# Kernel optimization log

Measured on AMD Instinct MI355X. Metric: run time of the kernel, lower is better.

## Reference

```python
import jax, jax.numpy as jnp
import numpy as np

B, CIN, H, W = 8, 128, 28, 28
COUT = 256
KH, KW, SH, SW, PH, PW = 3, 3, 1, 1, 1, 1
NCB, K = 64, 16
D = CIN * KH * KW          # 1152
SUB = D // NCB             # 18
OH = (H + 2 * PH - KH) // SH + 1
OW = (W + 2 * PW - KW) // SW + 1


def dequant(q, s, z):
    return (q.astype(jnp.float32) - z.astype(jnp.float32)) * s


def unfold(x):
    # x: (B, CIN, H, W) -> (B, D, OH*OW) with torch.unfold channel-major ordering
    xp = jnp.pad(x, ((0, 0), (0, 0), (PH, PH), (PW, PW)))
    patches = [xp[:, :, i:i + SH * OH:SH, j:j + SW * OW:SW]
               for i in range(KH) for j in range(KW)]
    cols = jnp.stack(patches, axis=2)  # (B, CIN, KH*KW, OH, OW)
    return cols.reshape(B, D, OH * OW)


def setup_inputs() -> dict:
    key = jax.random.key(0)
    ks = jax.random.split(key, 8)
    x_q = jax.random.randint(ks[0], (B, CIN, H, W), -128, 128, dtype=jnp.int32)
    x_s = jnp.array([0.02], jnp.float32)
    x_z = jnp.array([3], jnp.int32)
    centroids_q = jax.random.randint(ks[1], (NCB, K, SUB), -128, 128, dtype=jnp.int32)
    centroids_s = jax.random.uniform(ks[2], (NCB, 1, 1), jnp.float32) * 0.02 + 0.005
    centroids_z = jax.random.randint(ks[3], (NCB, 1, 1), -4, 5, dtype=jnp.int32)
    lut_q = jax.random.randint(ks[4], (NCB, K, COUT), -128, 128, dtype=jnp.int32)
    lut_s = jnp.array([0.015], jnp.float32)
    lut_z = jnp.array([1], jnp.int32)
    bias_q = jax.random.randint(ks[5], (COUT,), -1000, 1000, dtype=jnp.int32)
    bias_s = jnp.array([0.001], jnp.float32)
    bias_z = jnp.array([0], jnp.int32)
    output_s = jnp.array([0.05], jnp.float32)
    output_z = jnp.array([-2], jnp.int32)
    return dict(x_q=x_q, x_s=x_s, x_z=x_z,
                centroids_q=centroids_q, centroids_s=centroids_s, centroids_z=centroids_z,
                lut_q=lut_q, lut_s=lut_s, lut_z=lut_z,
                bias_q=bias_q, bias_s=bias_s, bias_z=bias_z,
                output_s=output_s, output_z=output_z)


def reference(x_q, x_s, x_z, centroids_q, centroids_s, centroids_z,
              lut_q, lut_s, lut_z, bias_q, bias_s, bias_z, output_s, output_z):
    x = dequant(x_q, x_s, x_z)                      # (B, CIN, H, W)
    cols = unfold(x)                                # (B, D, L)
    N = B * OH * OW
    # (B, L, D) -> (N, NCB, SUB) -> (NCB, N, SUB)
    xr = cols.transpose(0, 2, 1).reshape(N, NCB, SUB).transpose(1, 0, 2)
    c = dequant(centroids_q, centroids_s, centroids_z)  # (NCB, K, SUB)
    xy = jnp.einsum('cns,cks->cnk', xr, c)          # (NCB, N, K)
    y2 = jnp.sum(c * c, axis=-1)[:, None, :]        # (NCB, 1, K)
    den = x_s * centroids_s                         # (NCB, 1, 1)
    dist = -2.0 * jnp.round(xy / den) + jnp.round(y2 / den)
    idx = jnp.argmin(dist, axis=-1)                 # (NCB, N) int
    lut = dequant(lut_q, lut_s, lut_z)              # (NCB, K, COUT)
    # one_hot @ lut == gather rows of lut at idx, then sum over codebooks
    gathered = jnp.take_along_axis(lut, idx[:, :, None], axis=1)  # (NCB, N, COUT)
    out = jnp.sum(gathered, axis=0) + dequant(bias_q, bias_s, bias_z)  # (N, COUT)
    out = out.reshape(B, OH, OW, COUT).transpose(0, 3, 1, 2)
    out = jax.nn.relu(out)
    out_q = jnp.round(jnp.clip(out / output_s + output_z.astype(jnp.float32),
                               -128.0, 127.0)).astype(jnp.int8)
    return out_q
```

## Files before the change

kernel.cpp:

```cpp
#include <hip/hip_runtime.h>
#include <math.h>

constexpr int B_    = 8;
constexpr int CIN_  = 128;
constexpr int H_    = 28;
constexpr int W_    = 28;
constexpr int COUT_ = 256;
constexpr int OH_   = 28;
constexpr int OW_   = 28;
constexpr int L_    = OH_ * OW_;
constexpr int N_    = B_ * L_;
constexpr int NCB_  = 64;
constexpr int K_    = 16;
constexpr int SUB_  = 18;

constexpr size_t WS_IDX  = 0;
constexpr size_t WS_LUT8 = 0x100000;
constexpr size_t WS_BF2  = 0x180000;

__global__ __launch_bounds__(256, 2) void amm_k1(
    const int* __restrict__ x_q, const int* __restrict__ x_z,
    const int* __restrict__ c_q, const float* __restrict__ c_s,
    const int* __restrict__ c_z, const float* __restrict__ x_s,
    const int* __restrict__ lut_q, const float* __restrict__ lut_s,
    const int* __restrict__ lut_z,
    const int* __restrict__ bias_q, const float* __restrict__ bias_s,
    const int* __restrict__ bias_z,
    unsigned char* __restrict__ idx8, unsigned char* __restrict__ lut8,
    float* __restrict__ biasf2)
{
    const int bx  = blockIdx.x;
    const int tid = threadIdx.x;

    if (bx >= 512) {
        const int pb = bx - 512;
        if (pb < 256) {
            const int i = pb * 1024 + tid * 4;
            const int4 v = *(const int4*)(lut_q + i);
            uchar4 o;
            o.x = (unsigned char)(v.x + 128);
            o.y = (unsigned char)(v.y + 128);
            o.z = (unsigned char)(v.z + 128);
            o.w = (unsigned char)(v.w + 128);
            *(uchar4*)(lut8 + i) = o;
        } else {
            const double ls = (double)lut_s[0];
            const double c0 = (8192.0 + 64.0 * (double)lut_z[0]) * ls;
            biasf2[tid] = (float)((double)(bias_q[tid] - bias_z[0]) *
                                  (double)bias_s[0] - c0);
        }
        return;
    }

    const int cb = bx & 63;
    const int b  = bx >> 6;

    __shared__ float sx[2][900];
    __shared__ float c_lds[288];
    __shared__ float y2_lds[16];

    const int zc = c_z[cb];
    for (int i = tid; i < 1800; i += 256) ((float*)sx)[i] = 0.0f;
    for (int i = tid; i < 288; i += 256) {
        const int k = i / SUB_, s = i - k * SUB_;
        c_lds[s * 16 + k] = (float)(c_q[cb * 288 + i] - zc);
    }
    __syncthreads();

    const int xz = x_z[0];
    for (int i = tid; i < 2 * 784; i += 256) {
        const int c2 = i >= 784;
        const int r  = i - c2 * 784;
        const int h  = r / 28;
        const int w  = r - h * 28;
        sx[c2][(h + 1) * 30 + (w + 1)] =
            (float)(x_q[(size_t)(b * CIN_ + 2 * cb + c2) * L_ + r] - xz);
    }
    if (tid < 16) {
        const double csf = (double)c_s[cb];
        const double den = (double)x_s[0] * csf;
        double s2 = 0.0;
        for (int s = 0; s < SUB_; ++s) {
            const double d = (double)c_lds[s * 16 + tid] * csf;
            s2 += d * d;
        }
        y2_lds[tid] = (float)(int)rint(s2 / den);
    }
    __syncthreads();

    if (tid < 196) {
        float tap[4][SUB_];
        int   posr[4];
        #pragma unroll
        for (int ps = 0; ps < 4; ++ps) {
            const int p  = tid + 196 * ps;
            posr[ps] = p;
            const int oh = p / 28;
            const int ow = p - oh * 28;
            const int base = oh * 30 + ow;
            #pragma unroll
            for (int c2 = 0; c2 < 2; ++c2)
                #pragma unroll
                for (int kh = 0; kh < 3; ++kh)
                    #pragma unroll
                    for (int kw = 0; kw < 3; ++kw)
                        tap[ps][c2 * 9 + kh * 3 + kw] =
                            sx[c2][base + kh * 30 + kw];
        }

        float bestd[4] = {3.0e38f, 3.0e38f, 3.0e38f, 3.0e38f};
        int   bestk[4] = {0, 0, 0, 0};

        #pragma unroll
        for (int kc = 0; kc < 4; ++kc) {
            float acc[4][4];
            #pragma unroll
            for (int ps = 0; ps < 4; ++ps)
                #pragma unroll
                for (int kk = 0; kk < 4; ++kk) acc[ps][kk] = 0.0f;

            #pragma unroll
            for (int s = 0; s < SUB_; ++s) {
                const float4 c4 = *(const float4*)&c_lds[s * 16 + kc * 4];
                #pragma unroll
                for (int ps = 0; ps < 4; ++ps) {
                    const float xs = tap[ps][s];
                    acc[ps][0] = fmaf(xs, c4.x, acc[ps][0]);
                    acc[ps][1] = fmaf(xs, c4.y, acc[ps][1]);
                    acc[ps][2] = fmaf(xs, c4.z, acc[ps][2]);
                    acc[ps][3] = fmaf(xs, c4.w, acc[ps][3]);
                }
            }
            #pragma unroll
            for (int kk = 0; kk < 4; ++kk) {
                const float yk = y2_lds[kc * 4 + kk];
                #pragma unroll
                for (int ps = 0; ps < 4; ++ps) {
                    const float d = fmaf(-2.0f, acc[ps][kk], yk);
                    if (d < bestd[ps]) { bestd[ps] = d; bestk[ps] = kc * 4 + kk; }
                }
            }
        }

        unsigned char* op = idx8 + (size_t)cb * N_ + b * L_;
        #pragma unroll
        for (int ps = 0; ps < 4; ++ps)
            op[posr[ps]] = (unsigned char)bestk[ps];
    }
}

__global__ __launch_bounds__(256, 6) void amm_phase2(
    const unsigned char* __restrict__ idx8, const unsigned char* __restrict__ lut8,
    const float* __restrict__ lut_s, const float* __restrict__ biasf2,
    const float* __restrict__ out_s, const int* __restrict__ out_z,
    int* __restrict__ out)
{
    const int tid  = threadIdx.x;
    const int lane = tid & 63;
    const int wv   = __builtin_amdgcn_readfirstlane(tid >> 6);
    const int nb   = blockIdx.x * 4;
    const int b    = nb / L_;
    const int r0   = nb - b * L_;
    const int sh   = 8 * wv;

    __shared__ unsigned int sidx[64];
    __shared__ unsigned int res[4][132];

    if (tid < 64)
        sidx[tid] = *(const unsigned int*)(idx8 + (size_t)tid * N_ + nb);
    __syncthreads();

    const int cbq = lane >> 4;
    const int coq = lane & 15;

    unsigned int acc[8] = {0, 0, 0, 0, 0, 0, 0, 0};
    #pragma unroll
    for (int tb = 0; tb < 4; ++tb) {
        uint4 v[4];
        #pragma unroll
        for (int j = 0; j < 4; ++j) {
            const int cb = (tb * 4 + j) * 4 + cbq;
            const unsigned int k = (sidx[cb] >> sh) & 0xffu;
            v[j] = *(const uint4*)(lut8 + ((size_t)((cb << 4) + k) << 8)
                                        + (coq << 4));
        }
        #pragma unroll
        for (int j = 0; j < 4; ++j) {
            const unsigned int d[4] = {v[j].x, v[j].y, v[j].z, v[j].w};
            #pragma unroll
            for (int q = 0; q < 4; ++q) {
                acc[2 * q]     += d[q] & 0x00FF00FFu;
                acc[2 * q + 1] += (d[q] >> 8) & 0x00FF00FFu;
            }
        }
    }

    #pragma unroll
    for (int j = 0; j < 8; ++j) {
        acc[j] += __shfl_xor(acc[j], 16, 64);
        acc[j] += __shfl_xor(acc[j], 32, 64);
    }
    if (cbq == 0) {
        #pragma unroll
        for (int j = 0; j < 8; ++j) res[wv][coq * 8 + j] = acc[j];
    }
    __syncthreads();

    const float lsf = lut_s[0];
    const float osf = out_s[0];
    const float ozf = (float)out_z[0];

    const int co   = tid;
    const int u    = (co >> 4) * 8 + ((co & 15) >> 2) * 2 + (co & 1);
    const int half = (co >> 1) & 1;
    const float bf = biasf2[co];

    int4 ov;
    int* ovp = (int*)&ov;
    #pragma unroll
    for (int p = 0; p < 4; ++p) {
        const unsigned int vv = res[p][u];
        const int sv = (int)((vv >> (16 * half)) & 0xffffu);
        float f = (float)sv * lsf + bf;
        f = fmaxf(f, 0.0f) / osf + ozf;
        f = fminf(fmaxf(f, -128.0f), 127.0f);
        ovp[p] = (int)rintf(f);
    }
    *(int4*)(out + (size_t)(b * COUT_ + co) * L_ + r0) = ov;
}

extern "C" void kernel_launch(void* const* d_in, const int* in_sizes, int n_in,
                              void* d_out, int out_size, void* d_ws, size_t ws_size,
                              hipStream_t stream)
{
    const int*   x_q    = (const int*)  d_in[0];
    const float* x_s    = (const float*)d_in[1];
    const int*   x_z    = (const int*)  d_in[2];
    const int*   c_q    = (const int*)  d_in[3];
    const float* c_s    = (const float*)d_in[4];
    const int*   c_z    = (const int*)  d_in[5];
    const int*   lut_q  = (const int*)  d_in[6];
    const float* lut_s  = (const float*)d_in[7];
    const int*   lut_z  = (const int*)  d_in[8];
    const int*   bias_q = (const int*)  d_in[9];
    const float* bias_s = (const float*)d_in[10];
    const int*   bias_z = (const int*)  d_in[11];
    const float* out_s  = (const float*)d_in[12];
    const int*   out_z  = (const int*)  d_in[13];

    char* ws = (char*)d_ws;
    unsigned char* idx8 = (unsigned char*)(ws + WS_IDX);
    unsigned char* lut8 = (unsigned char*)(ws + WS_LUT8);
    float* biasf2 = (float*)(ws + WS_BF2);

    amm_k1<<<dim3(769), 256, 0, stream>>>(x_q, x_z, c_q, c_s, c_z, x_s,
                                          lut_q, lut_s, lut_z,
                                          bias_q, bias_s, bias_z,
                                          idx8, lut8, biasf2);

    amm_phase2<<<dim3(N_ / 4), 256, 0, stream>>>(
        idx8, lut8, lut_s, biasf2, out_s, out_z, (int*)d_out);
}
```

Measured before the change: 24.66 us.

## Fuse encode and LUT-accumulate phases into one cooperative kernel with grid sync

Merges the two kernel launches into a single cooperative kernel of 512 blocks. The first phase does LUT conversion, bias setup and per-codebook argmin encoding, then a grid-wide sync, then a grid-stride loop over output groups for the LUT gather-accumulate. This removes one launch and the gap between dependent kernels. In exchange it adds grid-sync cost and a fixed grid size, and falls back to the old two-kernel path if the cooperative launch fails.

```diff
diff --git a/kernel.cpp b/kernel.cpp
--- a/kernel.cpp
+++ b/kernel.cpp
@@ -1,22 +1,229 @@
 #include <hip/hip_runtime.h>
+#include <hip/hip_cooperative_groups.h>
 #include <math.h>
+
+namespace cg = cooperative_groups;
 
 constexpr int B_    = 8;
 constexpr int CIN_  = 128;
-constexpr int H_    = 28;
-constexpr int W_    = 28;
 constexpr int COUT_ = 256;
-constexpr int OH_   = 28;
-constexpr int OW_   = 28;
-constexpr int L_    = OH_ * OW_;
+constexpr int L_    = 784;
 constexpr int N_    = B_ * L_;
 constexpr int NCB_  = 64;
 constexpr int K_    = 16;
 constexpr int SUB_  = 18;
+constexpr int NGRP  = N_ / 4;
+constexpr int NBLK  = 512;
 
 constexpr size_t WS_IDX  = 0;
 constexpr size_t WS_LUT8 = 0x100000;
 constexpr size_t WS_BF2  = 0x180000;
+
+__global__ __launch_bounds__(256, 2) void amm_all(
+    const int* __restrict__ x_q, const int* __restrict__ x_z,
+    const int* __restrict__ c_q, const float* __restrict__ c_s,
+    const int* __restrict__ c_z, const float* __restrict__ x_s,
+    const int* __restrict__ lut_q, const float* __restrict__ lut_s,
+    const int* __restrict__ lut_z,
+    const int* __restrict__ bias_q, const float* __restrict__ bias_s,
+    const int* __restrict__ bias_z,
+    const float* __restrict__ out_s, const int* __restrict__ out_z,
+    unsigned char* __restrict__ idx8, unsigned char* __restrict__ lut8,
+    float* __restrict__ biasf2, int* __restrict__ out)
+{
+    const int bx  = blockIdx.x;
+    const int tid = threadIdx.x;
+
+    __shared__ float sx[2][900];
+    __shared__ float c_lds[288];
+    __shared__ float y2_lds[16];
+    __shared__ unsigned int sidx[64];
+    __shared__ unsigned int res[4][132];
+
+    if (tid < 128) {
+        const int i = (bx * 128 + tid) * 4;
+        const int4 v = *(const int4*)(lut_q + i);
+        uchar4 o;
+        o.x = (unsigned char)(v.x + 128);
+        o.y = (unsigned char)(v.y + 128);
+        o.z = (unsigned char)(v.z + 128);
+        o.w = (unsigned char)(v.w + 128);
+        *(uchar4*)(lut8 + i) = o;
+    }
+    if (bx == 0) {
+        const double ls = (double)lut_s[0];
+        const double c0 = (8192.0 + 64.0 * (double)lut_z[0]) * ls;
+        biasf2[tid] = (float)((double)(bias_q[tid] - bias_z[0]) *
+                              (double)bias_s[0] - c0);
+    }
+
+    {
+        const int cb = bx & 63;
+        const int b  = bx >> 6;
+
+        const int zc = c_z[cb];
+        for (int i = tid; i < 1800; i += 256) ((float*)sx)[i] = 0.0f;
+        for (int i = tid; i < 288; i += 256) {
+            const int k = i / SUB_, s = i - k * SUB_;
+            c_lds[s * 16 + k] = (float)(c_q[cb * 288 + i] - zc);
+        }
+        __syncthreads();
+
+        const int xz = x_z[0];
+        for (int i = tid; i < 2 * 784; i += 256) {
+            const int c2 = i >= 784;
+            const int r  = i - c2 * 784;
+            const int h  = r / 28;
+            const int w  = r - h * 28;
+            sx[c2][(h + 1) * 30 + (w + 1)] =
+                (float)(x_q[(size_t)(b * CIN_ + 2 * cb + c2) * L_ + r] - xz);
+        }
+        if (tid < 16) {
+            const double csf = (double)c_s[cb];
+            const double den = (double)x_s[0] * csf;
+            double s2 = 0.0;
+            for (int s = 0; s < SUB_; ++s) {
+                const double d = (double)c_lds[s * 16 + tid] * csf;
+                s2 += d * d;
+            }
+            y2_lds[tid] = (float)(int)rint(s2 / den);
+        }
+        __syncthreads();
+
+        if (tid < 196) {
+            float tap[4][SUB_];
+            int   posr[4];
+            #pragma unroll
+            for (int ps = 0; ps < 4; ++ps) {
+                const int p  = tid + 196 * ps;
+                posr[ps] = p;
+                const int oh = p / 28;
+                const int ow = p - oh * 28;
+                const int base = oh * 30 + ow;
+                #pragma unroll
+                for (int c2 = 0; c2 < 2; ++c2)
+                    #pragma unroll
+                    for (int kh = 0; kh < 3; ++kh)
+                        #pragma unroll
+                        for (int kw = 0; kw < 3; ++kw)
+                            tap[ps][c2 * 9 + kh * 3 + kw] =
+                                sx[c2][base + kh * 30 + kw];
+            }
+
+            float bestd[4] = {3.0e38f, 3.0e38f, 3.0e38f, 3.0e38f};
+            int   bestk[4] = {0, 0, 0, 0};
+
+            #pragma unroll
+            for (int kc = 0; kc < 4; ++kc) {
+                float acc[4][4];
+                #pragma unroll
+                for (int ps = 0; ps < 4; ++ps)
+                    #pragma unroll
+                    for (int kk = 0; kk < 4; ++kk) acc[ps][kk] = 0.0f;
+
+                #pragma unroll
+                for (int s = 0; s < SUB_; ++s) {
+                    const float4 c4 = *(const float4*)&c_lds[s * 16 + kc * 4];
+                    #pragma unroll
+                    for (int ps = 0; ps < 4; ++ps) {
+                        const float xs = tap[ps][s];
+                        acc[ps][0] = fmaf(xs, c4.x, acc[ps][0]);
+                        acc[ps][1] = fmaf(xs, c4.y, acc[ps][1]);
+                        acc[ps][2] = fmaf(xs, c4.z, acc[ps][2]);
+                        acc[ps][3] = fmaf(xs, c4.w, acc[ps][3]);
+                    }
+                }
+                #pragma unroll
+                for (int kk = 0; kk < 4; ++kk) {
+                    const float yk = y2_lds[kc * 4 + kk];
+                    #pragma unroll
+                    for (int ps = 0; ps < 4; ++ps) {
+                        const float d = fmaf(-2.0f, acc[ps][kk], yk);
+                        if (d < bestd[ps]) { bestd[ps] = d; bestk[ps] = kc * 4 + kk; }
+                    }
+                }
+            }
+
+            unsigned char* op = idx8 + (size_t)cb * N_ + b * L_;
+            #pragma unroll
+            for (int ps = 0; ps < 4; ++ps)
+                op[posr[ps]] = (unsigned char)bestk[ps];
+        }
+    }
+
+    cg::this_grid().sync();
+
+    const int lane = tid & 63;
+    const int wv   = __builtin_amdgcn_readfirstlane(tid >> 6);
+    const int sh   = 8 * wv;
+    const int cbq  = lane >> 4;
+    const int coq  = lane & 15;
+
+    const float lsf = lut_s[0];
+    const float osf = out_s[0];
+    const float ozf = (float)out_z[0];
+    const int co    = tid;
+    const int u     = (co >> 4) * 8 + ((co & 15) >> 2) * 2 + (co & 1);
+    const int half  = (co >> 1) & 1;
+    const float bf  = biasf2[co];
+
+    for (int g = bx; g < NGRP; g += NBLK) {
+        const int nb = g * 4;
+        const int b  = nb / L_;
+        const int r0 = nb - b * L_;
+
+        __syncthreads();
+        if (tid < 64)
+            sidx[tid] = *(const unsigned int*)(idx8 + (size_t)tid * N_ + nb);
+        __syncthreads();
+
+        unsigned int acc[8] = {0, 0, 0, 0, 0, 0, 0, 0};
+        #pragma unroll
+        for (int tb = 0; tb < 4; ++tb) {
+            uint4 v[4];
+            #pragma unroll
+            for (int j = 0; j < 4; ++j) {
+                const int cb = (tb * 4 + j) * 4 + cbq;
+                const unsigned int k = (sidx[cb] >> sh) & 0xffu;
+                v[j] = *(const uint4*)(lut8 + ((size_t)((cb << 4) + k) << 8)
+                                            + (coq << 4));
+            }
+            #pragma unroll
+            for (int j = 0; j < 4; ++j) {
+                const unsigned int d[4] = {v[j].x, v[j].y, v[j].z, v[j].w};
+                #pragma unroll
+                for (int q = 0; q < 4; ++q) {
+                    acc[2 * q]     += d[q] & 0x00FF00FFu;
+                    acc[2 * q + 1] += (d[q] >> 8) & 0x00FF00FFu;
+                }
+            }
+        }
+
+        #pragma unroll
+        for (int j = 0; j < 8; ++j) {
+            acc[j] += __shfl_xor(acc[j], 16, 64);
+            acc[j] += __shfl_xor(acc[j], 32, 64);
+        }
+        if (cbq == 0) {
+            #pragma unroll
+            for (int j = 0; j < 8; ++j) res[wv][coq * 8 + j] = acc[j];
+        }
+        __syncthreads();
+
+        int4 ov;
+        int* ovp = (int*)&ov;
+        #pragma unroll
+        for (int p = 0; p < 4; ++p) {
+            const unsigned int vv = res[p][u];
+            const int sv = (int)((vv >> (16 * half)) & 0xffffu);
+            float f = (float)sv * lsf + bf;
+            f = fmaxf(f, 0.0f) / osf + ozf;
+            f = fminf(fmaxf(f, -128.0f), 127.0f);
+            ovp[p] = (int)rintf(f);
+        }
+        *(int4*)(out + (size_t)(b * COUT_ + co) * L_ + r0) = ov;
+    }
+}
 
 __global__ __launch_bounds__(256, 2) void amm_k1(
     const int* __restrict__ x_q, const int* __restrict__ x_z,
@@ -252,12 +459,24 @@
     unsigned char* idx8 = (unsigned char*)(ws + WS_IDX);
     unsigned char* lut8 = (unsigned char*)(ws + WS_LUT8);
     float* biasf2 = (float*)(ws + WS_BF2);
-
-    amm_k1<<<dim3(769), 256, 0, stream>>>(x_q, x_z, c_q, c_s, c_z, x_s,
-                                          lut_q, lut_s, lut_z,
-                                          bias_q, bias_s, bias_z,
-                                          idx8, lut8, biasf2);
-
-    amm_phase2<<<dim3(N_ / 4), 256, 0, stream>>>(
-        idx8, lut8, lut_s, biasf2, out_s, out_z, (int*)d_out);
+    int* outp = (int*)d_out;
+
+    void* params[] = {
+        (void*)&x_q, (void*)&x_z, (void*)&c_q, (void*)&c_s, (void*)&c_z,
+        (void*)&x_s, (void*)&lut_q, (void*)&lut_s, (void*)&lut_z,
+        (void*)&bias_q, (void*)&bias_s, (void*)&bias_z,
+        (void*)&out_s, (void*)&out_z,
+        (void*)&idx8, (void*)&lut8, (void*)&biasf2, (void*)&outp,
+    };
+    const hipError_t e = hipLaunchCooperativeKernel(
+        (const void*)amm_all, dim3(NBLK), dim3(256), params, 0, stream);
+
+    if (e != hipSuccess) {
+        amm_k1<<<dim3(769), 256, 0, stream>>>(x_q, x_z, c_q, c_s, c_z, x_s,
+                                              lut_q, lut_s, lut_z,
+                                              bias_q, bias_s, bias_z,
+                                              idx8, lut8, biasf2);
+        amm_phase2<<<dim3(N_ / 4), 256, 0, stream>>>(
+            idx8, lut8, lut_s, biasf2, out_s, out_z, (int*)d_out);
+    }
 }
```

Result: slower. 77.51 us (+214.2%).
